# Optimization experiments

Hardware: AMD Instinct MI355X
Metric: run time of the kernel (lower is better)

Reference implementation:

```python
import math
import jax, jax.numpy as jnp
import numpy as np
from jax import lax

B, T, D = 2, 2048, 1024
H, W, E = 16, 16, 8
HD = D // H


def setup_inputs() -> dict:
    key = jax.random.key(0)
    ks = jax.random.split(key, 9)
    s = 0.02
    return {
        "x": jax.random.normal(ks[0], (B, T, D), dtype=jnp.float32),
        # CausalConv1d weights: torch Conv1d layout [out_ch, in_ch, kernel]
        "q_w": jax.random.normal(ks[1], (D, D, W), dtype=jnp.float32) * s,
        "q_b": jax.random.normal(ks[2], (D,), dtype=jnp.float32) * s,
        "k_w": jax.random.normal(ks[3], (D, D, W), dtype=jnp.float32) * s,
        "k_b": jax.random.normal(ks[4], (D,), dtype=jnp.float32) * s,
        # Linear weights: torch layout [out, in]
        "v_w": jax.random.normal(ks[5], (D, D), dtype=jnp.float32) * s,
        "v_b": jax.random.normal(ks[6], (D,), dtype=jnp.float32) * s,
        "p_w": jax.random.normal(ks[7], (D, D), dtype=jnp.float32) * s,
        "p_b": jax.random.normal(ks[8], (D,), dtype=jnp.float32) * s,
    }


def _causal_conv(x_t, w, b):
    # x_t: [B, D, T]; left-pad by W-1 so output at t sees inputs <= t
    xp = jnp.pad(x_t, ((0, 0), (0, 0), (W - 1, 0)))
    y = lax.conv_general_dilated(xp, w, window_strides=(1,), padding="VALID",
                                 dimension_numbers=("NCH", "OIH", "NCH"))
    return y + b[None, :, None]


def _split_heads(z):
    # [B, T, D] -> [B, H, T, hd]
    return z.reshape(B, T, H, HD).transpose(0, 2, 1, 3)


def reference(x, q_w, q_b, k_w, k_b, v_w, v_b, p_w, p_b):
    x_t = x.transpose(0, 2, 1)  # [B, D, T]
    q = _split_heads(_causal_conv(x_t, q_w, q_b).transpose(0, 2, 1))
    k = _split_heads(_causal_conv(x_t, k_w, k_b).transpose(0, 2, 1))
    v = _split_heads(jnp.einsum("btd,od->bto", x, v_w) + v_b)
    scale = 1.0 / math.sqrt(HD)

    # ---- local window attention (unfold equivalent) ----
    # zero-pad keys/values W-1 steps to the left along T, gather sliding windows
    k_pad = jnp.pad(k, ((0, 0), (0, 0), (W - 1, 0), (0, 0)))
    v_pad = jnp.pad(v, ((0, 0), (0, 0), (W - 1, 0), (0, 0)))
    widx = jnp.arange(T)[:, None] + jnp.arange(W)[None, :]  # [T, W]
    patches_k = k_pad[:, :, widx]  # [B, H, T, W, hd]
    patches_v = v_pad[:, :, widx]  # [B, H, T, W, hd]
    attn_l = jax.nn.softmax(jnp.einsum("bhtd,bhtwd->bhtw", q, patches_k) * scale, axis=-1)
    out_l = jnp.einsum("bhtw,bhtwd->bhtd", attn_l, patches_v)

    # ---- exponential jumps: roll by 2^e (wrap-around, as in original) ----
    out_e = jnp.zeros_like(out_l)
    for e in range(E):
        shift = 2 ** e
        if shift >= T:
            break
        k_s = jnp.roll(k, -shift, axis=2)
        v_s = jnp.roll(v, -shift, axis=2)
        score = jnp.sum(q * k_s, axis=-1) * scale  # [B, H, T]
        alpha = jax.nn.softmax(score, axis=-1)[..., None]  # softmax over T (faithful)
        out_e = out_e + alpha * v_s

    out = (out_l + out_e).transpose(0, 2, 1, 3).reshape(B, T, D)
    return jnp.einsum("btd,od->bto", out, p_w) + p_b
```

## Files before the change

### kernel.cpp

```cpp
#include <hip/hip_runtime.h>
#include <cstdint>
#include <cstddef>

#define TSEQ 2048
#define DDIM 1024

typedef _Float16 f16;
typedef _Float16 f16x2 __attribute__((ext_vector_type(2)));
typedef _Float16 f16x4 __attribute__((ext_vector_type(4)));
typedef _Float16 f16x8 __attribute__((ext_vector_type(8)));
typedef float f32x4 __attribute__((ext_vector_type(4)));


__device__ __align__(16) static const unsigned char g_zero16[16] = {};

__device__ __forceinline__ void gload_lds16(const void* g, void* l) {
  __builtin_amdgcn_global_load_lds(
      (const __attribute__((address_space(1))) void*)g,
      (__attribute__((address_space(3))) void*)l, 16, 0, 0);
}

__global__ void cvt_f32_f16(const float* __restrict__ src, f16* __restrict__ dst, int n4) {
  int i = blockIdx.x * 256 + threadIdx.x;
  if (i >= n4) return;
  float4 v = ((const float4*)src)[i];
  f16x4 h = { (f16)v.x, (f16)v.y, (f16)v.z, (f16)v.w };
  ((f16x4*)dst)[i] = h;
}

__global__ void cvt_w_transpose(const float* __restrict__ qw, const float* __restrict__ kw,
                                f16* __restrict__ qwh, f16* __restrict__ kwh) {
  __shared__ float tile[64 * 17];
  int o = blockIdx.x;
  const float* src;
  f16* dst;
  if (o < 1024) { src = qw + (size_t)o * 16384; dst = qwh + (size_t)o * 16384; }
  else          { src = kw + (size_t)(o - 1024) * 16384; dst = kwh + (size_t)(o - 1024) * 16384; }
  for (int i0 = 0; i0 < 1024; i0 += 64) {
    __syncthreads();
    #pragma unroll
    for (int p = 0; p < 4; p++) {
      int idx = p * 256 + threadIdx.x;
      float v = src[i0 * 16 + idx];
      tile[(idx >> 4) * 17 + (idx & 15)] = v;
    }
    __syncthreads();
    #pragma unroll
    for (int p = 0; p < 4; p++) {
      int idx = p * 256 + threadIdx.x;
      int w = idx >> 6, ii = idx & 63;
      dst[w * 1024 + i0 + ii] = (f16)tile[ii * 17 + w];
    }
  }
}

__global__ __launch_bounds__(256, 2) void gemm_qk(
    const f16* __restrict__ xh,
    const f16* __restrict__ Bq, const f16* __restrict__ Bk,
    const float* __restrict__ bq, const float* __restrict__ bk,
    f16* __restrict__ oq, f16* __restrict__ ok)
{
  __shared__ __align__(16) f16 smem[32768];
  const int tid = threadIdx.x;
  const int lane = tid & 63;
  const int wid = tid >> 6;
  const int wm = wid & 1;
  const int ks = wid >> 1;

  const int m0 = blockIdx.x * 128;
  const int n0 = blockIdx.y * 64;
  const int bT = m0 & ~(TSEQ - 1);
  const int t0 = m0 & (TSEQ - 1);

  const int srow = lane >> 3;
  const int scg = ((lane & 7) ^ ((lane >> 3) & 7)) * 8;

  f32x4 accq[4][4] = {};
  f32x4 acck[4][4] = {};

  const int slotoff = (((ks * 4 + (lane >> 4)) ^ (lane & 7)) * 8);

  auto stage = [&](int kk, int buf) {
    f16* sb = &smem[buf * 16384];
    if (wid < 2) {
      const int w = kk >> 10;
      const int i0 = (kk & (DDIM - 1)) + scg;
      #pragma unroll
      for (int c = 0; c < 8; c++) {
        const int s = wid * 8 + c;
        const int r = s * 8 + srow;
        const int srcT = t0 + r + w - 15;
        const void* g = (srcT >= 0)
            ? (const void*)(xh + (((size_t)(bT + srcT)) << 10) + i0)
            : (const void*)g_zero16;
        gload_lds16(g, (void*)&sb[s * 512]);
      }
    } else if (wid == 2) {
      #pragma unroll
      for (int c = 0; c < 8; c++) {
        const int r = c * 8 + srow;
        const void* g = (const void*)(Bq + ((size_t)(n0 + r) << 14) + kk + scg);
        gload_lds16(g, (void*)&sb[8192 + c * 512]);
      }
    } else {
      #pragma unroll
      for (int c = 0; c < 8; c++) {
        const int r = c * 8 + srow;
        const void* g = (const void*)(Bk + ((size_t)(n0 + r) << 14) + kk + scg);
        gload_lds16(g, (void*)&sb[12288 + c * 512]);
      }
    }
  };

  stage(0, 0);
  for (int kk = 0; kk < 16384; kk += 64) {
    const int buf = (kk >> 6) & 1;
    __syncthreads();
    if (kk + 64 < 16384) stage(kk + 64, buf ^ 1);

    const f16* sb = &smem[buf * 16384];
    f16x8 af[4], bfq[4], bfk[4];
    #pragma unroll
    for (int i = 0; i < 4; i++) {
      const int r = wm * 64 + i * 16 + (lane & 15);
      af[i] = *(const f16x8*)&sb[r * 64 + slotoff];
    }
    #pragma unroll
    for (int j = 0; j < 4; j++) {
      const int r = j * 16 + (lane & 15);
      bfq[j] = *(const f16x8*)&sb[8192 + r * 64 + slotoff];
      bfk[j] = *(const f16x8*)&sb[12288 + r * 64 + slotoff];
    }
    #pragma unroll
    for (int i = 0; i < 4; i++)
      #pragma unroll
      for (int j = 0; j < 4; j++) {
        accq[i][j] = __builtin_amdgcn_mfma_f32_16x16x32_f16(af[i], bfq[j], accq[i][j], 0, 0, 0);
        acck[i][j] = __builtin_amdgcn_mfma_f32_16x16x32_f16(af[i], bfk[j], acck[i][j], 0, 0, 0);
      }
  }

  const int crow = (lane >> 4) * 4;
  const int ccol = lane & 15;
  const int hh = n0 >> 6;
  float* red = (float*)smem + wm * 4096;

  __syncthreads();
  if (ks == 1) {
    #pragma unroll
    for (int i = 0; i < 4; i++)
      #pragma unroll
      for (int j = 0; j < 4; j++)
        #pragma unroll
        for (int r = 0; r < 4; r++)
          red[(i * 16 + crow + r) * 64 + j * 16 + ccol] = accq[i][j][r];
  }
  __syncthreads();
  if (ks == 0) {
    #pragma unroll
    for (int j = 0; j < 4; j++) {
      const int col = n0 + j * 16 + ccol;
      const float bvl = bq[col];
      const int d = j * 16 + ccol;
      #pragma unroll
      for (int i = 0; i < 4; i++)
        #pragma unroll
        for (int r = 0; r < 4; r++) {
          const int row = m0 + wm * 64 + i * 16 + crow + r;
          const int b = row >> 11, t = row & (TSEQ - 1);
          const float v = accq[i][j][r] + red[(i * 16 + crow + r) * 64 + j * 16 + ccol] + bvl;
          oq[((size_t)(b * 16 + hh) * TSEQ + t) * 64 + d] = (f16)v;
        }
    }
  }
  __syncthreads();
  if (ks == 1) {
    #pragma unroll
    for (int i = 0; i < 4; i++)
      #pragma unroll
      for (int j = 0; j < 4; j++)
        #pragma unroll
        for (int r = 0; r < 4; r++)
          red[(i * 16 + crow + r) * 64 + j * 16 + ccol] = acck[i][j][r];
  }
  __syncthreads();
  if (ks == 0) {
    #pragma unroll
    for (int j = 0; j < 4; j++) {
      const int col = n0 + j * 16 + ccol;
      const float bvl = bk[col];
      const int d = j * 16 + ccol;
      #pragma unroll
      for (int i = 0; i < 4; i++)
        #pragma unroll
        for (int r = 0; r < 4; r++) {
          const int row = m0 + wm * 64 + i * 16 + crow + r;
          const int b = row >> 11, t = row & (TSEQ - 1);
          const float v = acck[i][j][r] + red[(i * 16 + crow + r) * 64 + j * 16 + ccol] + bvl;
          ok[((size_t)(b * 16 + hh) * TSEQ + t) * 64 + d] = (f16)v;
        }
    }
  }
}

template<int MODE>
__global__ __launch_bounds__(256, 2) void gemm_small(
    const f16* __restrict__ A, const f16* __restrict__ Bw,
    const float* __restrict__ bias, f16* __restrict__ oh, float* __restrict__ ofp)
{
  __shared__ f16 As[128 * 32];
  __shared__ f16 Bs[128 * 32];
  const int tid = threadIdx.x;
  const int lane = tid & 63;
  const int wid = tid >> 6;
  const int m0 = blockIdx.x * 128;
  const int n0 = blockIdx.y * 128;

  const int srow = lane >> 2;
  const int scg = ((lane & 3) ^ ((lane >> 3) & 3)) * 8;
  const int wm = wid & 1;
  const int wn = wid >> 1;

  f32x4 acc[4][4] = {};

  for (int kk = 0; kk < 1024; kk += 32) {
    __syncthreads();
    if (wid < 2) {
      #pragma unroll
      for (int c = 0; c < 4; c++) {
        const int r = wid * 64 + c * 16 + srow;
        const void* g = (const void*)(A + (((size_t)(m0 + r)) << 10) + kk + scg);
        gload_lds16(g, (void*)&As[(wid * 64 + c * 16) * 32]);
      }
    } else {
      #pragma unroll
      for (int c = 0; c < 4; c++) {
        const int r = (wid - 2) * 64 + c * 16 + srow;
        const void* g = (const void*)(Bw + (((size_t)(n0 + r)) << 10) + kk + scg);
        gload_lds16(g, (void*)&Bs[((wid - 2) * 64 + c * 16) * 32]);
      }
    }
    __syncthreads();
    const int koff = ((lane >> 4) ^ ((lane >> 1) & 3)) * 8;
    f16x8 af[4], bf[4];
    #pragma unroll
    for (int i = 0; i < 4; i++) {
      af[i] = *(const f16x8*)&As[(wm * 64 + i * 16 + (lane & 15)) * 32 + koff];
      bf[i] = *(const f16x8*)&Bs[(wn * 64 + i * 16 + (lane & 15)) * 32 + koff];
    }
    #pragma unroll
    for (int i = 0; i < 4; i++)
      #pragma unroll
      for (int j = 0; j < 4; j++)
        acc[i][j] = __builtin_amdgcn_mfma_f32_16x16x32_f16(af[i], bf[j], acc[i][j], 0, 0, 0);
  }

  const int crow = (lane >> 4) * 4;
  const int ccol = lane & 15;
  #pragma unroll
  for (int j = 0; j < 4; j++) {
    const int col = n0 + wn * 64 + j * 16 + ccol;
    const float bvl = bias[col];
    #pragma unroll
    for (int i = 0; i < 4; i++) {
      #pragma unroll
      for (int r = 0; r < 4; r++) {
        const int row = m0 + wm * 64 + i * 16 + crow + r;
        const float val = acc[i][j][r] + bvl;
        if (MODE == 1) {
          ofp[(size_t)row * DDIM + col] = val;
        } else {
          const int b = row >> 11, t = row & (TSEQ - 1);
          const int h = col >> 6, d = col & 63;
          oh[((size_t)(b * 16 + h) * TSEQ + t) * 64 + d] = (f16)val;
        }
      }
    }
  }
}

__global__ __launch_bounds__(256) void score_k(const f16* __restrict__ qh,
                                               const f16* __restrict__ kh,
                                               float* __restrict__ scores) {
  const int bid = blockIdx.x;
  const int bh = bid >> 3, tc = bid & 7;
  const int tid = threadIdx.x;
  const int wave = tid >> 6, lane = tid & 63;
  const int tr = lane >> 3, dc = lane & 7;
  const size_t base = ((size_t)bh) << 17;
  const f16* qb = qh + base;
  const f16* kb = kh + base;

  #pragma unroll
  for (int p = 0; p < 8; p++) {
    const int t = tc * 256 + wave * 64 + p * 8 + tr;
    f16x8 qv = *(const f16x8*)(qb + (size_t)t * 64 + dc * 8);
    const f16x2* qp = (const f16x2*)&qv;
    #pragma unroll
    for (int e = 0; e < 8; e++) {
      const int ts = (t + (1 << e)) & (TSEQ - 1);
      f16x8 kv = *(const f16x8*)(kb + (size_t)ts * 64 + dc * 8);
      const f16x2* kp = (const f16x2*)&kv;
      float s = 0.f;
      #pragma unroll
      for (int j = 0; j < 4; j++) s = __builtin_amdgcn_fdot2(qp[j], kp[j], s, false);
      s += __shfl_xor(s, 1, 64);
      s += __shfl_xor(s, 2, 64);
      s += __shfl_xor(s, 4, 64);
      if (dc == 0) scores[((size_t)(bh * 8 + e) << 11) + t] = s * 0.125f;
    }
  }
}

__global__ void softmax_k(float* __restrict__ scores) {
  __shared__ float red[4];
  int row = blockIdx.x;
  float* p = scores + ((size_t)row << 11);
  int tid = threadIdx.x;
  float v[8];
  float4 a = ((const float4*)p)[tid * 2];
  float4 b = ((const float4*)p)[tid * 2 + 1];
  v[0] = a.x; v[1] = a.y; v[2] = a.z; v[3] = a.w;
  v[4] = b.x; v[5] = b.y; v[6] = b.z; v[7] = b.w;
  float m = v[0];
  #pragma unroll
  for (int j = 1; j < 8; j++) m = fmaxf(m, v[j]);
  for (int o = 32; o > 0; o >>= 1) m = fmaxf(m, __shfl_xor(m, o, 64));
  if ((tid & 63) == 0) red[tid >> 6] = m;
  __syncthreads();
  m = fmaxf(fmaxf(red[0], red[1]), fmaxf(red[2], red[3]));
  __syncthreads();
  float s = 0.f;
  #pragma unroll
  for (int j = 0; j < 8; j++) { v[j] = __expf(v[j] - m); s += v[j]; }
  for (int o = 32; o > 0; o >>= 1) s += __shfl_xor(s, o, 64);
  if ((tid & 63) == 0) red[tid >> 6] = s;
  __syncthreads();
  s = (red[0] + red[1]) + (red[2] + red[3]);
  float inv = 1.0f / s;
  float4 o1 = make_float4(v[0] * inv, v[1] * inv, v[2] * inv, v[3] * inv);
  float4 o2 = make_float4(v[4] * inv, v[5] * inv, v[6] * inv, v[7] * inv);
  ((float4*)p)[tid * 2] = o1;
  ((float4*)p)[tid * 2 + 1] = o2;
}

__global__ __launch_bounds__(256) void attn_out_k(
    const f16* __restrict__ qh, const f16* __restrict__ kh, const f16* __restrict__ vh,
    const float* __restrict__ alpha, f16* __restrict__ outh)
{
  __shared__ f16 qL[64 * 64];
  __shared__ f16 kL[80 * 64];
  __shared__ f16 vL[208 * 64];
  __shared__ float scL[64 * 16];
  __shared__ float aL[8 * 64];
  const int bh = blockIdx.x, tc = blockIdx.y;
  const int t0 = tc * 64;
  const int tid = threadIdx.x;
  const size_t base = ((size_t)bh) << 17;

  for (int idx = tid; idx < 64 * 8; idx += 256) {
    int r = idx >> 3, c = idx & 7, sl = c ^ (r & 7);
    *(uint4*)&qL[r * 64 + sl * 8] = *(const uint4*)(qh + base + (size_t)(t0 + r) * 64 + c * 8);
  }
  for (int idx = tid; idx < 79 * 8; idx += 256) {
    int r = idx >> 3, c = idx & 7, sl = c ^ (r & 7);
    int g = t0 - 15 + r;
    uint4 val = (g < 0) ? make_uint4(0, 0, 0, 0)
                        : *(const uint4*)(kh + base + (size_t)g * 64 + c * 8);
    *(uint4*)&kL[r * 64 + sl * 8] = val;
  }
  for (int idx = tid; idx < 207 * 8; idx += 256) {
    int r = idx >> 3, c = idx & 7, sl = c ^ (r & 7);
    int g = t0 - 15 + r;
    uint4 val;
    if (g < 0) val = make_uint4(0, 0, 0, 0);
    else {
      if (g >= TSEQ) g -= TSEQ;
      val = *(const uint4*)(vh + base + (size_t)g * 64 + c * 8);
    }
    *(uint4*)&vL[r * 64 + sl * 8] = val;
  }
  for (int idx = tid; idx < 512; idx += 256) {
    int e = idx >> 6, i = idx & 63;
    aL[e * 64 + i] = alpha[((size_t)(bh * 8 + e) << 11) + t0 + i];
  }
  __syncthreads();

  {
    const int tl = tid & 63;
    const int wg = tid >> 6;
    f16x8 qv[8];
    #pragma unroll
    for (int c = 0; c < 8; c++) qv[c] = *(const f16x8*)&qL[tl * 64 + ((c ^ (tl & 7)) * 8)];
    const f16x2* qp = (const f16x2*)&qv[0];
    #pragma unroll
    for (int wi = 0; wi < 4; wi++) {
      const int w = wg * 4 + wi;
      const int r = tl + w;
      float s = 0.f;
      #pragma unroll
      for (int c = 0; c < 8; c++) {
        f16x8 kv = *(const f16x8*)&kL[r * 64 + ((c ^ (r & 7)) * 8)];
        const f16x2* kp = (const f16x2*)&kv;
        #pragma unroll
        for (int j = 0; j < 4; j++) s = __builtin_amdgcn_fdot2(qp[c * 4 + j], kp[j], s, false);
      }
      scL[tl * 16 + w] = s * 0.125f;
    }
  }
  __syncthreads();

  if (tid < 64) {
    float sc[16];
    float m = -1e30f;
    #pragma unroll
    for (int w = 0; w < 16; w++) { sc[w] = scL[tid * 16 + w]; m = fmaxf(m, sc[w]); }
    float sum = 0.f;
    #pragma unroll
    for (int w = 0; w < 16; w++) { sc[w] = __expf(sc[w] - m); sum += sc[w]; }
    float inv = 1.0f / sum;
    #pragma unroll
    for (int w = 0; w < 16; w++) scL[tid * 16 + w] = sc[w] * inv;
  }
  __syncthreads();

  {
    const int tl = tid >> 2;
    const int qd = tid & 3;
    float accv[16] = {};
    #pragma unroll
    for (int w = 0; w < 16; w++) {
      const float pw_ = scL[tl * 16 + w];
      const int r = tl + w;
      #pragma unroll
      for (int c2 = 0; c2 < 2; c2++) {
        const int c = qd * 2 + c2;
        f16x8 v = *(const f16x8*)&vL[r * 64 + ((c ^ (r & 7)) * 8)];
        #pragma unroll
        for (int j = 0; j < 8; j++) accv[c2 * 8 + j] += pw_ * (float)v[j];
      }
    }
    #pragma unroll
    for (int e = 0; e < 8; e++) {
      const float a = aL[e * 64 + tl];
      const int r = tl + 15 + (1 << e);
      #pragma unroll
      for (int c2 = 0; c2 < 2; c2++) {
        const int c = qd * 2 + c2;
        f16x8 v = *(const f16x8*)&vL[r * 64 + ((c ^ (r & 7)) * 8)];
        #pragma unroll
        for (int j = 0; j < 8; j++) accv[c2 * 8 + j] += a * (float)v[j];
      }
    }
    const int b = bh >> 4, h = bh & 15;
    f16* orow = outh + ((size_t)(b * TSEQ + t0 + tl)) * DDIM + h * 64 + qd * 16;
    #pragma unroll
    for (int c2 = 0; c2 < 2; c2++) {
      f16x8 v;
      #pragma unroll
      for (int j = 0; j < 8; j++) v[j] = (f16)accv[c2 * 8 + j];
      *(f16x8*)(orow + c2 * 8) = v;
    }
  }
}

extern "C" void kernel_launch(void* const* d_in, const int* in_sizes, int n_in,
                              void* d_out, int out_size, void* d_ws, size_t ws_size,
                              hipStream_t stream) {
  (void)in_sizes; (void)n_in; (void)out_size; (void)ws_size;
  const float* x   = (const float*)d_in[0];
  const float* q_w = (const float*)d_in[1];
  const float* q_b = (const float*)d_in[2];
  const float* k_w = (const float*)d_in[3];
  const float* k_b = (const float*)d_in[4];
  const float* v_w = (const float*)d_in[5];
  const float* v_b = (const float*)d_in[6];
  const float* p_w = (const float*)d_in[7];
  const float* p_b = (const float*)d_in[8];
  float* out = (float*)d_out;

  char* ws = (char*)d_ws;
  f16* xh      = (f16*)(ws);
  f16* qwh     = (f16*)(ws + 8388608);
  f16* kwh     = (f16*)(ws + 41943040);
  f16* vwh     = (f16*)(ws + 75497472);
  f16* pwh     = (f16*)(ws + 77594624);
  f16* qh      = (f16*)(ws + 79691776);
  f16* kh      = (f16*)(ws + 88080384);
  f16* vh      = (f16*)(ws + 96468992);
  f16* outh    = (f16*)(ws + 104857600);
  float* alpha = (float*)(ws + 113246208);

  cvt_f32_f16<<<4096, 256, 0, stream>>>(x, xh, 1048576);
  cvt_f32_f16<<<1024, 256, 0, stream>>>(v_w, vwh, 262144);
  cvt_f32_f16<<<1024, 256, 0, stream>>>(p_w, pwh, 262144);
  cvt_w_transpose<<<2048, 256, 0, stream>>>(q_w, k_w, qwh, kwh);

  gemm_qk<<<dim3(32, 16), 256, 0, stream>>>(xh, qwh, kwh, q_b, k_b, qh, kh);
  gemm_small<0><<<dim3(32, 8), 256, 0, stream>>>(xh, vwh, v_b, vh, nullptr);

  score_k<<<256, 256, 0, stream>>>(qh, kh, alpha);
  softmax_k<<<256, 256, 0, stream>>>(alpha);
  attn_out_k<<<dim3(32, 32), 256, 0, stream>>>(qh, kh, vh, alpha, outh);

  gemm_small<1><<<dim3(32, 8), 256, 0, stream>>>(outh, pwh, p_b, nullptr, out);
}
```

Measured before the change: 546.1 us.

## Pre-pack conv weights in MFMA fragment order and load B directly to registers

The conv weight conversion now writes q/k weights in a fragment-major layout, so gemm_qk can load B operands straight from global memory into registers with coalesced 16-byte loads. LDS then only stages the A (shifted x) tile, which halves shared memory use, and the main loop is unrolled by two with register double-buffered B fragments. The three f32-to-f16 conversion launches are merged into one kernel, and score_k is split across four times as many blocks to raise parallelism. The risks are extra register pressure from the B fragment buffers and global-load latency that is no longer hidden behind LDS staging.

```diff
diff --git a/kernel.cpp b/kernel.cpp
--- a/kernel.cpp
+++ b/kernel.cpp
@@ -20,37 +20,63 @@
       (__attribute__((address_space(3))) void*)l, 16, 0, 0);
 }
 
-__global__ void cvt_f32_f16(const float* __restrict__ src, f16* __restrict__ dst, int n4) {
-  int i = blockIdx.x * 256 + threadIdx.x;
-  if (i >= n4) return;
+__global__ void cvt_all(const float* __restrict__ x, const float* __restrict__ vw,
+                        const float* __restrict__ pw,
+                        f16* __restrict__ xh, f16* __restrict__ vwh, f16* __restrict__ pwh) {
+  int b = blockIdx.x;
+  const float* src; f16* dst; int i;
+  if (b < 4096)      { src = x;  dst = xh;  i = b * 256 + threadIdx.x; }
+  else if (b < 5120) { src = vw; dst = vwh; i = (b - 4096) * 256 + threadIdx.x; }
+  else               { src = pw; dst = pwh; i = (b - 5120) * 256 + threadIdx.x; }
   float4 v = ((const float4*)src)[i];
   f16x4 h = { (f16)v.x, (f16)v.y, (f16)v.z, (f16)v.w };
   ((f16x4*)dst)[i] = h;
 }
 
-__global__ void cvt_w_transpose(const float* __restrict__ qw, const float* __restrict__ kw,
-                                f16* __restrict__ qwh, f16* __restrict__ kwh) {
-  __shared__ float tile[64 * 17];
-  int o = blockIdx.x;
-  const float* src;
-  f16* dst;
-  if (o < 1024) { src = qw + (size_t)o * 16384; dst = qwh + (size_t)o * 16384; }
-  else          { src = kw + (size_t)(o - 1024) * 16384; dst = kwh + (size_t)(o - 1024) * 16384; }
-  for (int i0 = 0; i0 < 1024; i0 += 64) {
-    __syncthreads();
-    #pragma unroll
-    for (int p = 0; p < 4; p++) {
-      int idx = p * 256 + threadIdx.x;
-      float v = src[i0 * 16 + idx];
-      tile[(idx >> 4) * 17 + (idx & 15)] = v;
-    }
-    __syncthreads();
-    #pragma unroll
-    for (int p = 0; p < 4; p++) {
-      int idx = p * 256 + threadIdx.x;
-      int w = idx >> 6, ii = idx & 63;
-      dst[w * 1024 + i0 + ii] = (f16)tile[ii * 17 + w];
-    }
+__global__ __launch_bounds__(256) void cvt_w_frag(const float* __restrict__ qw,
+                                                  const float* __restrict__ kw,
+                                                  f16* __restrict__ qd, f16* __restrict__ kd) {
+  __shared__ __align__(16) f16 tile[16 * 1160];
+  const int bid = blockIdx.x;
+  const float* src = (bid < 1024) ? qw : kw;
+  f16* dst = (bid < 1024) ? qd : kd;
+  const int bb = bid & 1023;
+  const int o_tile = bb >> 4;
+  const int ib = bb & 15;
+  const int i0 = ib * 64;
+  const int tid = threadIdx.x;
+
+  #pragma unroll
+  for (int p = 0; p < 2; p++) {
+    const int o_l = p * 8 + (tid >> 5);
+    const int sub = tid & 31;
+    const int io = sub >> 2;
+    const int wq = sub & 3;
+    const float* s = src + (size_t)(o_tile * 16 + o_l) * 16384 + (size_t)(i0 + io * 8) * 16 + wq * 4;
+    float4 v[8];
+    #pragma unroll
+    for (int r = 0; r < 8; r++) v[r] = *(const float4*)(s + r * 16);
+    f16* t = &tile[o_l * 1160 + io * 8];
+    #pragma unroll
+    for (int j = 0; j < 4; j++) {
+      f16x8 hv;
+      #pragma unroll
+      for (int r = 0; r < 8; r++) hv[r] = (f16)((&v[r].x)[j]);
+      *(f16x8*)&t[(wq * 4 + j) * 72] = hv;
+    }
+  }
+  __syncthreads();
+  #pragma unroll
+  for (int p = 0; p < 8; p++) {
+    const int c = p * 256 + tid;
+    const int w = c >> 7;
+    const int ksub = (c >> 6) & 1;
+    const int l = c & 63;
+    const int o_l = l & 15;
+    const int i_local = ksub * 32 + ((l >> 4) << 3);
+    f16x8 v = *(const f16x8*)&tile[o_l * 1160 + w * 72 + i_local];
+    const int kc = w * 32 + ib * 2 + ksub;
+    *(f16x8*)(dst + ((size_t)(o_tile * 512 + kc)) * 512 + l * 8) = v;
   }
 }
 
@@ -60,7 +86,7 @@
     const float* __restrict__ bq, const float* __restrict__ bk,
     f16* __restrict__ oq, f16* __restrict__ ok)
 {
-  __shared__ __align__(16) f16 smem[32768];
+  __shared__ __align__(16) f16 smem[16384];
   const int tid = threadIdx.x;
   const int lane = tid & 63;
   const int wid = tid >> 6;
@@ -79,65 +105,58 @@
   f32x4 acck[4][4] = {};
 
   const int slotoff = (((ks * 4 + (lane >> 4)) ^ (lane & 7)) * 8);
-
-  auto stage = [&](int kk, int buf) {
-    f16* sb = &smem[buf * 16384];
-    if (wid < 2) {
-      const int w = kk >> 10;
-      const int i0 = (kk & (DDIM - 1)) + scg;
-      #pragma unroll
-      for (int c = 0; c < 8; c++) {
-        const int s = wid * 8 + c;
-        const int r = s * 8 + srow;
-        const int srcT = t0 + r + w - 15;
-        const void* g = (srcT >= 0)
-            ? (const void*)(xh + (((size_t)(bT + srcT)) << 10) + i0)
-            : (const void*)g_zero16;
-        gload_lds16(g, (void*)&sb[s * 512]);
-      }
-    } else if (wid == 2) {
-      #pragma unroll
-      for (int c = 0; c < 8; c++) {
-        const int r = c * 8 + srow;
-        const void* g = (const void*)(Bq + ((size_t)(n0 + r) << 14) + kk + scg);
-        gload_lds16(g, (void*)&sb[8192 + c * 512]);
-      }
-    } else {
-      #pragma unroll
-      for (int c = 0; c < 8; c++) {
-        const int r = c * 8 + srow;
-        const void* g = (const void*)(Bk + ((size_t)(n0 + r) << 14) + kk + scg);
-        gload_lds16(g, (void*)&sb[12288 + c * 512]);
-      }
+  const size_t bbase = (size_t)(n0 >> 4) * 512 * 512 + (size_t)lane * 8;
+
+  auto stageA = [&](int kk, int buf) {
+    f16* sb = &smem[buf * 8192];
+    const int w = kk >> 10;
+    const int i0 = (kk & (DDIM - 1)) + scg;
+    #pragma unroll
+    for (int c = 0; c < 4; c++) {
+      const int s = wid * 4 + c;
+      const int r = s * 8 + srow;
+      const int srcT = t0 + r + w - 15;
+      const void* g = (srcT >= 0)
+          ? (const void*)(xh + (((size_t)(bT + srcT)) << 10) + i0)
+          : (const void*)g_zero16;
+      gload_lds16(g, (void*)&sb[s * 512]);
     }
   };
-
-  stage(0, 0);
-  for (int kk = 0; kk < 16384; kk += 64) {
-    const int buf = (kk >> 6) & 1;
-    __syncthreads();
-    if (kk + 64 < 16384) stage(kk + 64, buf ^ 1);
-
-    const f16* sb = &smem[buf * 16384];
-    f16x8 af[4], bfq[4], bfk[4];
+  auto loadB = [&](int kk, f16x8* q, f16x8* k) {
+    const int kc = (kk >> 5) + ks;
+    #pragma unroll
+    for (int j = 0; j < 4; j++) {
+      q[j] = *(const f16x8*)(Bq + bbase + ((size_t)(j * 512 + kc)) * 512);
+      k[j] = *(const f16x8*)(Bk + bbase + ((size_t)(j * 512 + kc)) * 512);
+    }
+  };
+  auto compute = [&](const f16* sb, const f16x8* bqf, const f16x8* bkf) {
+    f16x8 af[4];
     #pragma unroll
     for (int i = 0; i < 4; i++) {
       const int r = wm * 64 + i * 16 + (lane & 15);
       af[i] = *(const f16x8*)&sb[r * 64 + slotoff];
     }
     #pragma unroll
-    for (int j = 0; j < 4; j++) {
-      const int r = j * 16 + (lane & 15);
-      bfq[j] = *(const f16x8*)&sb[8192 + r * 64 + slotoff];
-      bfk[j] = *(const f16x8*)&sb[12288 + r * 64 + slotoff];
-    }
-    #pragma unroll
     for (int i = 0; i < 4; i++)
       #pragma unroll
       for (int j = 0; j < 4; j++) {
-        accq[i][j] = __builtin_amdgcn_mfma_f32_16x16x32_f16(af[i], bfq[j], accq[i][j], 0, 0, 0);
-        acck[i][j] = __builtin_amdgcn_mfma_f32_16x16x32_f16(af[i], bfk[j], acck[i][j], 0, 0, 0);
-      }
+        accq[i][j] = __builtin_amdgcn_mfma_f32_16x16x32_f16(af[i], bqf[j], accq[i][j], 0, 0, 0);
+        acck[i][j] = __builtin_amdgcn_mfma_f32_16x16x32_f16(af[i], bkf[j], acck[i][j], 0, 0, 0);
+      }
+  };
+
+  f16x8 bq0[4], bk0[4], bq1[4], bk1[4];
+  stageA(0, 0);
+  loadB(0, bq0, bk0);
+  for (int kk = 0; kk < 16384; kk += 128) {
+    __syncthreads();
+    stageA(kk + 64, 1);
+    loadB(kk + 64, bq1, bk1);
+    compute(&smem[0], bq0, bk0);
+    __syncthreads();
+    if (kk + 128 < 16384) { stageA(kk + 128, 0); loadB(kk + 128, bq0, bk0); }
+    compute(&smem[8192], bq1, bk1);
   }
 
   const int crow = (lane >> 4) * 4;
@@ -283,7 +302,7 @@
                                                const f16* __restrict__ kh,
                                                float* __restrict__ scores) {
   const int bid = blockIdx.x;
-  const int bh = bid >> 3, tc = bid & 7;
+  const int bh = bid >> 5, tc = bid & 31;
   const int tid = threadIdx.x;
   const int wave = tid >> 6, lane = tid & 63;
   const int tr = lane >> 3, dc = lane & 7;
@@ -292,8 +311,8 @@
   const f16* kb = kh + base;
 
   #pragma unroll
-  for (int p = 0; p < 8; p++) {
-    const int t = tc * 256 + wave * 64 + p * 8 + tr;
+  for (int p = 0; p < 2; p++) {
+    const int t = tc * 64 + p * 32 + wave * 8 + tr;
     f16x8 qv = *(const f16x8*)(qb + (size_t)t * 64 + dc * 8);
     const f16x2* qp = (const f16x2*)&qv;
     #pragma unroll
@@ -491,15 +510,13 @@
   f16* outh    = (f16*)(ws + 104857600);
   float* alpha = (float*)(ws + 113246208);
 
-  cvt_f32_f16<<<4096, 256, 0, stream>>>(x, xh, 1048576);
-  cvt_f32_f16<<<1024, 256, 0, stream>>>(v_w, vwh, 262144);
-  cvt_f32_f16<<<1024, 256, 0, stream>>>(p_w, pwh, 262144);
-  cvt_w_transpose<<<2048, 256, 0, stream>>>(q_w, k_w, qwh, kwh);
+  cvt_all<<<6144, 256, 0, stream>>>(x, v_w, p_w, xh, vwh, pwh);
+  cvt_w_frag<<<2048, 256, 0, stream>>>(q_w, k_w, qwh, kwh);
 
   gemm_qk<<<dim3(32, 16), 256, 0, stream>>>(xh, qwh, kwh, q_b, k_b, qh, kh);
   gemm_small<0><<<dim3(32, 8), 256, 0, stream>>>(xh, vwh, v_b, vh, nullptr);
 
-  score_k<<<256, 256, 0, stream>>>(qh, kh, alpha);
+  score_k<<<1024, 256, 0, stream>>>(qh, kh, alpha);
   softmax_k<<<256, 256, 0, stream>>>(alpha);
   attn_out_k<<<dim3(32, 32), 256, 0, stream>>>(qh, kh, vh, alpha, outh);
 
```

Result: no change. 549.1 us (+0.5%).
